# Optimization experiments

Measured on AMD Instinct MI355X. Metric: run time of the kernel, lower is better.

The kernel has to match this reference:

```python
import jax, jax.numpy as jnp
import numpy as np

NUM_CHARS = 26  # hardcoded in original module


def setup_inputs() -> dict:
    key = jax.random.key(0)
    ks = jax.random.split(key, 8)
    B, T, H = 2048, 1024, NUM_CHARS
    s = 1.0 / np.sqrt(H)
    return {
        "x": jax.random.randint(ks[0], (B, T), 0, NUM_CHARS, dtype=jnp.int64),
        "E": jax.random.normal(ks[1], (NUM_CHARS, H), dtype=jnp.float32),            # embedding table
        "W_ih": jax.random.uniform(ks[2], (4 * H, H), jnp.float32, -s, s),           # LSTM input weights (i,f,g,o)
        "W_hh": jax.random.uniform(ks[3], (4 * H, H), jnp.float32, -s, s),           # LSTM hidden weights
        "b_ih": jax.random.uniform(ks[4], (4 * H,), jnp.float32, -s, s),
        "b_hh": jax.random.uniform(ks[5], (4 * H,), jnp.float32, -s, s),
        "W_lin": jax.random.uniform(ks[6], (NUM_CHARS, H), jnp.float32, -s, s),      # final Linear weight
        "b_lin": jax.random.uniform(ks[7], (NUM_CHARS,), jnp.float32, -s, s),
    }


def reference(x, E, W_ih, W_hh, b_ih, b_hh, W_lin, b_lin):
    # Embedding lookup: [B,T] -> [B,T,H]
    emb = E[x]
    B, T, H = emb.shape
    # Precompute input projections for all timesteps: [B,T,4H]
    x_proj = jnp.einsum('bth,gh->btg', emb, W_ih) + b_ih

    def step(carry, xt):  # xt: [B,4H]
        h, c = carry
        gates = xt + h @ W_hh.T + b_hh  # [B,4H], torch gate order i,f,g,o
        i, f, g, o = jnp.split(gates, 4, axis=-1)
        i = jax.nn.sigmoid(i)
        f = jax.nn.sigmoid(f)
        g = jnp.tanh(g)
        o = jax.nn.sigmoid(o)
        c = f * c + i * g
        h = o * jnp.tanh(c)
        return (h, c), None

    h0 = jnp.zeros((B, H), emb.dtype)
    (hT, _), _ = jax.lax.scan(step, (h0, h0), jnp.swapaxes(x_proj, 0, 1))
    # h_n has shape [num_layers=1, B, H]; .squeeze(1) is a no-op for B>1
    out = hT @ W_lin.T + b_lin  # [B,26]
    return out[None]  # [1,B,26]
```

## Files before the change

### kernel.cpp

```cpp
#include <hip/hip_runtime.h>

#define LOG2E 1.442695040888963f

typedef float f32x2 __attribute__((ext_vector_type(2)));
typedef float f32x4 __attribute__((ext_vector_type(4)));

static __device__ __forceinline__ void pkfma(f32x2& acc, f32x2 a, f32x2 b) {
    asm("v_pk_fma_f32 %0, %1, %2, %0" : "+v"(acc) : "v"(a), "v"(b));
}
static __device__ __forceinline__ void pkmul(f32x2& d, f32x2 a, f32x2 b) {
    asm("v_pk_mul_f32 %0, %1, %2" : "=v"(d) : "v"(a), "v"(b));
}

__launch_bounds__(64, 2)
__global__ void lstm_char_kernel(const int* __restrict__ x,
                                 const float* __restrict__ E,
                                 const float* __restrict__ W_ih,
                                 const float* __restrict__ W_hh,
                                 const float* __restrict__ b_ih,
                                 const float* __restrict__ b_hh,
                                 const float* __restrict__ W_lin,
                                 const float* __restrict__ b_lin,
                                 float* __restrict__ out,
                                 int T)
{
    constexpr int H = 26;

    __shared__ __align__(16) f32x2 P[26][64];
    __shared__ float Ebuf[676];
    __shared__ int   chars[1026];
    __shared__ __align__(16) float hbuf[64];

    const int b = blockIdx.x;
    const int l = threadIdx.x;
    const int j = l & 31;
    const bool lo = (l < 32);
    const int rr = (j < 26) ? j : 0;
    const int r0 = lo ? rr : 26 + rr;
    const int r1 = lo ? 52 + rr : 78 + rr;

    for (int i = l; i < 676; i += 64) Ebuf[i] = E[i];
    for (int t = l; t < T; t += 64) chars[t] = x[(size_t)b * T + t] * 512;
    if (l < 2) chars[1024 + l] = 0;
    hbuf[l] = 0.0f;

    const float m0 = -LOG2E;
    const float m1 = lo ? (-2.0f * LOG2E) : (-LOG2E);
    const float s1 = lo ? (-4.0f * LOG2E) : 1.0f;
    const float d1 = lo ? ( 2.0f * LOG2E) : 0.0f;

    f32x2 wh0p[13], wh1p[13];
    #pragma unroll
    for (int k = 0; k < 13; ++k) {
        wh0p[k] = f32x2{W_hh[r0 * H + 2 * k] * m0, W_hh[r0 * H + 2 * k + 1] * m0};
        wh1p[k] = f32x2{W_hh[r1 * H + 2 * k] * m1, W_hh[r1 * H + 2 * k + 1] * m1};
    }

    {
        float wi0[H], wi1[H];
        #pragma unroll
        for (int k = 0; k < H; ++k) {
            wi0[k] = W_ih[r0 * H + k];
            wi1[k] = W_ih[r1 * H + k];
        }
        const float bias0 = b_ih[r0] + b_hh[r0];
        const float bias1 = b_ih[r1] + b_hh[r1];
        __syncthreads();
        for (int ch = 0; ch < 26; ++ch) {
            float a0 = bias0, a1 = bias1;
            #pragma unroll
            for (int k = 0; k < H; ++k) {
                float e = Ebuf[ch * H + k];
                a0 = fmaf(wi0[k], e, a0);
                a1 = fmaf(wi1[k], e, a1);
            }
            P[ch][l] = f32x2{a0 * m0, a1 * m1};
        }
    }
    __syncthreads();

    const int hidx = (l - 32) & 63;
    const char* Pb = (const char*)&P[0][0];
    const int lane8 = l << 3;

    int poffn = chars[1];
    f32x2 pa = *(const f32x2*)(Pb + chars[0] + lane8);
    float C = 0.0f;

    #pragma unroll 2
    for (int t = 0; t < T; ++t) {
        f32x4 hv4[7];
        #pragma unroll
        for (int q = 0; q < 7; ++q) hv4[q] = ((const f32x4*)hbuf)[q];
        f32x2 hp[13];
        #pragma unroll
        for (int q = 0; q < 6; ++q) {
            hp[2 * q]     = f32x2{hv4[q].x, hv4[q].y};
            hp[2 * q + 1] = f32x2{hv4[q].z, hv4[q].w};
        }
        hp[12] = f32x2{hv4[6].x, hv4[6].y};

        f32x2 pn = *(const f32x2*)(Pb + poffn + lane8);
        int poff2 = chars[t + 2];

        f32x2 A0, A1, B0, B1;
        pkmul(A0, hp[0], wh0p[0]);
        pkmul(A1, hp[1], wh0p[1]);
        pkmul(B0, hp[0], wh1p[0]);
        pkmul(B1, hp[1], wh1p[1]);
        #pragma unroll
        for (int k = 2; k < 12; k += 2) {
            pkfma(A0, hp[k],     wh0p[k]);
            pkfma(A1, hp[k + 1], wh0p[k + 1]);
            pkfma(B0, hp[k],     wh1p[k]);
            pkfma(B1, hp[k + 1], wh1p[k + 1]);
        }
        pkfma(A0, hp[12], wh0p[12]);
        pkfma(B0, hp[12], wh1p[12]);
        f32x2 sa = A0 + A1;
        f32x2 sb = B0 + B1;
        const float a0s = sa.x + sa.y + pa.x;
        const float a1s = sb.x + sb.y + pa.y;

        float y0 = __builtin_amdgcn_rcpf(1.0f + __builtin_amdgcn_exp2f(a0s));
        float y1 = fmaf(__builtin_amdgcn_rcpf(1.0f + __builtin_amdgcn_exp2f(a1s)),
                        s1, d1);
        float y1_2 = y1 + y1;
        float ny1  = -y1;

        float pr = y0 * y1;
        auto sw = __builtin_amdgcn_permlane32_swap(__float_as_int(pr),
                                                   __float_as_int(pr),
                                                   false, false);
        float rcv = (__int_as_float(sw[0]) + __int_as_float(sw[1])) - pr;

        C = fmaf(y0, C, rcv);
        float rc = __builtin_amdgcn_rcpf(1.0f + __builtin_amdgcn_exp2f(C));
        float hv = fmaf(rc, y1_2, ny1);
        hbuf[hidx] = hv;

        pa = pn; poffn = poff2;
    }

    __syncthreads();

    if (l < H) {
        float acc = b_lin[l];
        #pragma unroll
        for (int k = 0; k < H; ++k)
            acc = fmaf(W_lin[l * H + k], hbuf[k], acc);
        out[(size_t)b * H + l] = acc;
    }
}

extern "C" void kernel_launch(void* const* d_in, const int* in_sizes, int n_in,
                              void* d_out, int out_size, void* d_ws, size_t ws_size,
                              hipStream_t stream) {
    const int*   x     = (const int*)d_in[0];
    const float* E     = (const float*)d_in[1];
    const float* W_ih  = (const float*)d_in[2];
    const float* W_hh  = (const float*)d_in[3];
    const float* b_ih  = (const float*)d_in[4];
    const float* b_hh  = (const float*)d_in[5];
    const float* W_lin = (const float*)d_in[6];
    const float* b_lin = (const float*)d_in[7];
    float* out = (float*)d_out;

    const int T = 1024;
    const int B = in_sizes[0] / T;

    lstm_char_kernel<<<B, 64, 0, stream>>>(x, E, W_ih, W_hh, b_ih, b_hh,
                                           W_lin, b_lin, out, T);
}
```

Baseline: 285.1 us.

## Drop E staging, use 16-bit char offsets, stagger blocks, simplify lane swap

The embedding table is now read straight from global memory during the input-projection precompute, so the shared Ebuf and one barrier go away. Character offsets are stored as 16-bit values in shared memory. A per-block hash-based busy-wait of reciprocal instructions is inserted before the recurrence, to desynchronize blocks sharing a CU. The hidden-state reads change from f32x4 loads to f32x2 loads, and the cross-half exchange now passes y0 as the permlane32_swap old operand and takes one result directly instead of add-and-subtract. The delay adds idle work, and the new swap operand semantics are a correctness risk if the half-wave mapping is wrong.

```diff
diff --git a/kernel.cpp b/kernel.cpp
--- a/kernel.cpp
+++ b/kernel.cpp
@@ -3,7 +3,6 @@
 #define LOG2E 1.442695040888963f
 
 typedef float f32x2 __attribute__((ext_vector_type(2)));
-typedef float f32x4 __attribute__((ext_vector_type(4)));
 
 static __device__ __forceinline__ void pkfma(f32x2& acc, f32x2 a, f32x2 b) {
     asm("v_pk_fma_f32 %0, %1, %2, %0" : "+v"(acc) : "v"(a), "v"(b));
@@ -27,8 +26,7 @@
     constexpr int H = 26;
 
     __shared__ __align__(16) f32x2 P[26][64];
-    __shared__ float Ebuf[676];
-    __shared__ int   chars[1026];
+    __shared__ __align__(8) unsigned short chars[1032];
     __shared__ __align__(16) float hbuf[64];
 
     const int b = blockIdx.x;
@@ -39,9 +37,9 @@
     const int r0 = lo ? rr : 26 + rr;
     const int r1 = lo ? 52 + rr : 78 + rr;
 
-    for (int i = l; i < 676; i += 64) Ebuf[i] = E[i];
-    for (int t = l; t < T; t += 64) chars[t] = x[(size_t)b * T + t] * 512;
-    if (l < 2) chars[1024 + l] = 0;
+    for (int t = l; t < T; t += 64)
+        chars[t] = (unsigned short)(x[(size_t)b * T + t] * 512);
+    if (l < 8) chars[1024 + l] = 0;
     hbuf[l] = 0.0f;
 
     const float m0 = -LOG2E;
@@ -65,12 +63,11 @@
         }
         const float bias0 = b_ih[r0] + b_hh[r0];
         const float bias1 = b_ih[r1] + b_hh[r1];
-        __syncthreads();
         for (int ch = 0; ch < 26; ++ch) {
             float a0 = bias0, a1 = bias1;
             #pragma unroll
             for (int k = 0; k < H; ++k) {
-                float e = Ebuf[ch * H + k];
+                float e = E[ch * H + k];
                 a0 = fmaf(wi0[k], e, a0);
                 a1 = fmaf(wi1[k], e, a1);
             }
@@ -79,26 +76,31 @@
     }
     __syncthreads();
 
+    {
+        unsigned hsh = (blockIdx.x * 2654435761u) >> 29;
+        float dch = (float)(l + 1);
+        for (unsigned i = 0; i < hsh; ++i) {
+            asm volatile("v_rcp_f32 %0, %0\n\t"
+                         "v_rcp_f32 %0, %0\n\t"
+                         "v_rcp_f32 %0, %0\n\t"
+                         "v_rcp_f32 %0, %0" : "+v"(dch));
+        }
+        asm volatile("" :: "v"(dch));
+    }
+
     const int hidx = (l - 32) & 63;
     const char* Pb = (const char*)&P[0][0];
     const int lane8 = l << 3;
 
     int poffn = chars[1];
-    f32x2 pa = *(const f32x2*)(Pb + chars[0] + lane8);
+    f32x2 pa = *(const f32x2*)(Pb + (int)chars[0] + lane8);
     float C = 0.0f;
 
     #pragma unroll 2
     for (int t = 0; t < T; ++t) {
-        f32x4 hv4[7];
-        #pragma unroll
-        for (int q = 0; q < 7; ++q) hv4[q] = ((const f32x4*)hbuf)[q];
         f32x2 hp[13];
         #pragma unroll
-        for (int q = 0; q < 6; ++q) {
-            hp[2 * q]     = f32x2{hv4[q].x, hv4[q].y};
-            hp[2 * q + 1] = f32x2{hv4[q].z, hv4[q].w};
-        }
-        hp[12] = f32x2{hv4[6].x, hv4[6].y};
+        for (int q = 0; q < 13; ++q) hp[q] = ((const f32x2*)hbuf)[q];
 
         f32x2 pn = *(const f32x2*)(Pb + poffn + lane8);
         int poff2 = chars[t + 2];
@@ -126,17 +128,16 @@
         float y1 = fmaf(__builtin_amdgcn_rcpf(1.0f + __builtin_amdgcn_exp2f(a1s)),
                         s1, d1);
         float y1_2 = y1 + y1;
-        float ny1  = -y1;
 
         float pr = y0 * y1;
-        auto sw = __builtin_amdgcn_permlane32_swap(__float_as_int(pr),
+        auto sw = __builtin_amdgcn_permlane32_swap(__float_as_int(y0),
                                                    __float_as_int(pr),
                                                    false, false);
-        float rcv = (__int_as_float(sw[0]) + __int_as_float(sw[1])) - pr;
+        float rcv = __int_as_float(sw[0]);
 
         C = fmaf(y0, C, rcv);
         float rc = __builtin_amdgcn_rcpf(1.0f + __builtin_amdgcn_exp2f(C));
-        float hv = fmaf(rc, y1_2, ny1);
+        float hv = fmaf(rc, y1_2, -y1);
         hbuf[hidx] = hv;
 
         pa = pn; poffn = poff2;
```

Measured after the change: 276.3 us. -3.1%, faster.
